# Optimization experiments

Measured on AMD Instinct MI355X. Metric: run time of the kernel, lower is better.

The kernel has to match this reference:

```python
import jax, jax.numpy as jnp
import numpy as np

D_MODEL = 512
NHEAD = 8
HEAD_DIM = D_MODEL // NHEAD
A, B = 1024, 16


def setup_inputs() -> dict:
    key = jax.random.key(0)
    ks = jax.random.split(key, 6)
    s = 1.0 / np.sqrt(D_MODEL)
    return {
        "src": jax.random.normal(ks[0], (A, B, D_MODEL), jnp.float32),
        "asset_relation_bias": jax.random.normal(ks[1], (A, A), jnp.float32) * 0.1,
        "Wq": jax.random.normal(ks[2], (D_MODEL, D_MODEL), jnp.float32) * s,
        "bq": jnp.zeros((D_MODEL,), jnp.float32),
        "Wk": jax.random.normal(ks[3], (D_MODEL, D_MODEL), jnp.float32) * s,
        "bk": jnp.zeros((D_MODEL,), jnp.float32),
        "Wv": jax.random.normal(ks[4], (D_MODEL, D_MODEL), jnp.float32) * s,
        "bv": jnp.zeros((D_MODEL,), jnp.float32),
        "Wo": jax.random.normal(ks[5], (D_MODEL, D_MODEL), jnp.float32) * s,
        "bo": jnp.zeros((D_MODEL,), jnp.float32),
    }


def reference(src, asset_relation_bias, Wq, bq, Wk, bk, Wv, bv, Wo, bo):
    # src: [A, B, H]; attention is over the asset dim A.
    scale = HEAD_DIM ** -0.5

    def proj_heads(x, W, b):
        y = x @ W.T + b                      # [A, B, H]  (torch Linear: x @ W.T + b)
        y = y.reshape(A, B, NHEAD, HEAD_DIM)
        return jnp.transpose(y, (1, 2, 0, 3))  # [B, nh, A, hd]

    q = proj_heads(src, Wq, bq)
    k = proj_heads(src, Wk, bk)
    v = proj_heads(src, Wv, bv)

    logits = jnp.einsum("bnad,bnkd->bnak", q, k) * scale  # [B, nh, A, A]
    logits = logits + asset_relation_bias[None, None]     # additive relation bias
    attn = jax.nn.softmax(logits, axis=-1)                # dropout = identity (eval)
    out = jnp.einsum("bnak,bnkd->bnad", attn, v)          # [B, nh, A, hd]
    out = jnp.transpose(out, (2, 0, 1, 3)).reshape(A, B, D_MODEL)
    out = out @ Wo.T + bo
    return out
```

## Files before the change

kernel.cpp:

```cpp
#include <hip/hip_runtime.h>
#include <hip/hip_bf16.h>

#define A_DIM 1024
#define B_DIM 16
#define DM    512
#define NH    8
#define HD    64

#define LDT 72

typedef short s16x8 __attribute__((ext_vector_type(8)));
typedef float f32x4 __attribute__((ext_vector_type(4)));

static __device__ __forceinline__ unsigned short f2b(float f) {
    __hip_bfloat16 h = __float2bfloat16(f);
    unsigned short u;
    __builtin_memcpy(&u, &h, 2);
    return u;
}
static __device__ __forceinline__ uint2 cvt4(float4 v) {
    __hip_bfloat162 lo = __float22bfloat162_rn(make_float2(v.x, v.y));
    __hip_bfloat162 hi = __float22bfloat162_rn(make_float2(v.z, v.w));
    unsigned int ulo, uhi;
    __builtin_memcpy(&ulo, &lo, 4);
    __builtin_memcpy(&uhi, &hi, 4);
    return make_uint2(ulo, uhi);
}

__global__ __launch_bounds__(256) void qkv_gemm(
    const float* __restrict__ src,
    const float* __restrict__ Wq, const float* __restrict__ bq,
    const float* __restrict__ Wk, const float* __restrict__ bk,
    const float* __restrict__ Wv, const float* __restrict__ bv,
    short* __restrict__ Qb, short* __restrict__ Kb, short* __restrict__ Vb)
{
    __shared__ short As[128 * LDT];
    __shared__ short Bs[128 * LDT];

    const int tid  = threadIdx.x;
    const int wave = tid >> 6, lane = tid & 63;
    const int quad = lane >> 4, l16 = lane & 15;
    const int waveM = (wave >> 1) * 64, waveN = (wave & 1) * 64;
    const int mbase = blockIdx.y * 128;
    const int nbase = blockIdx.x * 128;
    const int mat   = nbase >> 9;
    const float* W    = (mat == 0) ? Wq : (mat == 1) ? Wk : Wv;
    const float* bvec = (mat == 0) ? bq : (mat == 1) ? bk : bv;
    short* dst        = (mat == 0) ? Qb : (mat == 1) ? Kb : Vb;
    const float oscale = (mat == 0) ? 0.125f : 1.0f;
    const int wrow0 = nbase & 511;

    f32x4 acc[4][4];
    #pragma unroll
    for (int i = 0; i < 4; i++)
        #pragma unroll
        for (int j = 0; j < 4; j++)
            acc[i][j] = (f32x4){0.f, 0.f, 0.f, 0.f};

    for (int kb = 0; kb < 8; ++kb) {
        __syncthreads();
        #pragma unroll
        for (int p = 0; p < 8; p++) {
            int chunk = tid + p * 256;
            int row = chunk >> 4, c = chunk & 15;
            float4 a4 = *(const float4*)&src[(mbase + row) * 512 + kb * 64 + c * 4];
            *(uint2*)&As[row * LDT + c * 4] = cvt4(a4);
            float4 w4 = *(const float4*)&W[(wrow0 + row) * 512 + kb * 64 + c * 4];
            *(uint2*)&Bs[row * LDT + c * 4] = cvt4(w4);
        }
        __syncthreads();
        #pragma unroll
        for (int k0i = 0; k0i < 2; k0i++) {
            s16x8 af[4], bf[4];
            #pragma unroll
            for (int mi = 0; mi < 4; mi++)
                af[mi] = *(const s16x8*)&As[(waveM + mi * 16 + l16) * LDT + (k0i * 4 + quad) * 8];
            #pragma unroll
            for (int ni = 0; ni < 4; ni++)
                bf[ni] = *(const s16x8*)&Bs[(waveN + ni * 16 + l16) * LDT + (k0i * 4 + quad) * 8];
            #pragma unroll
            for (int mi = 0; mi < 4; mi++)
                #pragma unroll
                for (int ni = 0; ni < 4; ni++)
                    acc[mi][ni] = __builtin_amdgcn_mfma_f32_16x16x32_bf16(
                        af[mi], bf[ni], acc[mi][ni], 0, 0, 0);
        }
    }

    #pragma unroll
    for (int mi = 0; mi < 4; mi++) {
        #pragma unroll
        for (int ni = 0; ni < 4; ni++) {
            #pragma unroll
            for (int r = 0; r < 4; r++) {
                int t = mbase + waveM + mi * 16 + quad * 4 + r;
                int o = wrow0 + waveN + ni * 16 + l16;
                float v = (acc[mi][ni][r] + bvec[o]) * oscale;
                int a = t >> 4, bb = t & 15, n = o >> 6, d = o & 63;
                dst[((bb * NH + n) * A_DIM + a) * HD + d] = (short)f2b(v);
            }
        }
    }
}

__global__ __launch_bounds__(256) void attn_kernel(
    const short* __restrict__ Qb, const short* __restrict__ Kb,
    const short* __restrict__ Vb, const float* __restrict__ bias,
    short* __restrict__ AO)
{
    __shared__ short Ks[64 * LDT];
    __shared__ short Vt[64 * LDT];
    __shared__ short Ps[4][16 * LDT];

    const int tid  = threadIdx.x;
    const int wave = tid >> 6, lane = tid & 63;
    const int quad = lane >> 4, l16 = lane & 15;
    const int bn = blockIdx.y;
    const int qrow0 = blockIdx.x * 64 + wave * 16;

    const short* Qg = Qb + bn * (A_DIM * HD);
    const short* Kg = Kb + bn * (A_DIM * HD);
    const short* Vg = Vb + bn * (A_DIM * HD);

    s16x8 qf[2];
    #pragma unroll
    for (int k0i = 0; k0i < 2; k0i++)
        qf[k0i] = *(const s16x8*)&Qg[(qrow0 + l16) * HD + k0i * 32 + quad * 8];

    float lsum[4];
    f32x4 of[4];
    #pragma unroll
    for (int r = 0; r < 4; r++) lsum[r] = 0.f;
    #pragma unroll
    for (int db = 0; db < 4; db++) of[db] = (f32x4){0.f, 0.f, 0.f, 0.f};

    for (int kb = 0; kb < 16; ++kb) {
        __syncthreads();
        #pragma unroll
        for (int p = 0; p < 2; p++) {
            int chunk = tid + p * 256;
            int row = chunk >> 3, c = chunk & 7;
            *(s16x8*)&Ks[row * LDT + c * 8] =
                *(const s16x8*)&Kg[(kb * 64 + row) * HD + c * 8];
            s16x8 vv = *(const s16x8*)&Vg[(kb * 64 + row) * HD + c * 8];
            #pragma unroll
            for (int j = 0; j < 8; j++) {
                int d = c * 8 + j;
                Vt[d * LDT + (((row >> 3) ^ c) << 3) + (row & 7)] = vv[j];
            }
        }
        __syncthreads();

        float sv[4][4];
        #pragma unroll
        for (int cb = 0; cb < 4; cb++) {
            f32x4 s = (f32x4){0.f, 0.f, 0.f, 0.f};
            #pragma unroll
            for (int k0i = 0; k0i < 2; k0i++) {
                s16x8 kf = *(const s16x8*)&Ks[(cb * 16 + l16) * LDT + (k0i * 4 + quad) * 8];
                s = __builtin_amdgcn_mfma_f32_16x16x32_bf16(qf[k0i], kf, s, 0, 0, 0);
            }
            #pragma unroll
            for (int r = 0; r < 4; r++) {
                int arow = qrow0 + quad * 4 + r;
                int kcol = kb * 64 + cb * 16 + l16;
                sv[cb][r] = s[r] + bias[arow * A_DIM + kcol];
            }
        }

        #pragma unroll
        for (int r = 0; r < 4; r++) {
            int prow = quad * 4 + r;
            #pragma unroll
            for (int cb = 0; cb < 4; cb++) {
                float pv = __expf(sv[cb][r]);
                lsum[r] += pv;
                Ps[wave][prow * LDT + cb * 16 + l16] = (short)f2b(pv);
            }
        }

        #pragma unroll
        for (int k0i = 0; k0i < 2; k0i++) {
            s16x8 pf = *(const s16x8*)&Ps[wave][l16 * LDT + (k0i * 4 + quad) * 8];
            #pragma unroll
            for (int db = 0; db < 4; db++) {
                int rr = db * 16 + l16;
                s16x8 vf = *(const s16x8*)&Vt[rr * LDT +
                            (((k0i * 4 + quad) ^ (rr >> 3)) << 3)];
                of[db] = __builtin_amdgcn_mfma_f32_16x16x32_bf16(pf, vf, of[db], 0, 0, 0);
            }
        }
    }

    #pragma unroll
    for (int r = 0; r < 4; r++) {
        float ps = lsum[r];
        ps += __shfl_xor(ps, 1);
        ps += __shfl_xor(ps, 2);
        ps += __shfl_xor(ps, 4);
        ps += __shfl_xor(ps, 8);
        lsum[r] = 1.0f / ps;
    }

    const int b = bn >> 3, n = bn & 7;
    #pragma unroll
    for (int db = 0; db < 4; db++) {
        #pragma unroll
        for (int r = 0; r < 4; r++) {
            int a = qrow0 + quad * 4 + r;
            int d = db * 16 + l16;
            float v = of[db][r] * lsum[r];
            AO[(a * B_DIM + b) * DM + n * HD + d] = (short)f2b(v);
        }
    }
}

__global__ __launch_bounds__(256) void out_gemm(
    const short* __restrict__ Xin,
    const float* __restrict__ Wo, const float* __restrict__ bo,
    float* __restrict__ out)
{
    __shared__ short As[128 * LDT];
    __shared__ short Bs[128 * LDT];

    const int tid  = threadIdx.x;
    const int wave = tid >> 6, lane = tid & 63;
    const int quad = lane >> 4, l16 = lane & 15;
    const int waveM = (wave >> 1) * 64, waveN = (wave & 1) * 64;
    const int mbase = blockIdx.y * 128;
    const int nbase = blockIdx.x * 128;

    f32x4 acc[4][4];
    #pragma unroll
    for (int i = 0; i < 4; i++)
        #pragma unroll
        for (int j = 0; j < 4; j++)
            acc[i][j] = (f32x4){0.f, 0.f, 0.f, 0.f};

    for (int kb = 0; kb < 8; ++kb) {
        __syncthreads();
        #pragma unroll
        for (int p = 0; p < 4; p++) {
            int chunk = tid + p * 256;
            int row = chunk >> 3, c = chunk & 7;
            *(s16x8*)&As[row * LDT + c * 8] =
                *(const s16x8*)&Xin[(mbase + row) * 512 + kb * 64 + c * 8];
        }
        #pragma unroll
        for (int p = 0; p < 8; p++) {
            int chunk = tid + p * 256;
            int row = chunk >> 4, c = chunk & 15;
            float4 w4 = *(const float4*)&Wo[(nbase + row) * 512 + kb * 64 + c * 4];
            *(uint2*)&Bs[row * LDT + c * 4] = cvt4(w4);
        }
        __syncthreads();
        #pragma unroll
        for (int k0i = 0; k0i < 2; k0i++) {
            s16x8 af[4], bf[4];
            #pragma unroll
            for (int mi = 0; mi < 4; mi++)
                af[mi] = *(const s16x8*)&As[(waveM + mi * 16 + l16) * LDT + (k0i * 4 + quad) * 8];
            #pragma unroll
            for (int ni = 0; ni < 4; ni++)
                bf[ni] = *(const s16x8*)&Bs[(waveN + ni * 16 + l16) * LDT + (k0i * 4 + quad) * 8];
            #pragma unroll
            for (int mi = 0; mi < 4; mi++)
                #pragma unroll
                for (int ni = 0; ni < 4; ni++)
                    acc[mi][ni] = __builtin_amdgcn_mfma_f32_16x16x32_bf16(
                        af[mi], bf[ni], acc[mi][ni], 0, 0, 0);
        }
    }

    #pragma unroll
    for (int mi = 0; mi < 4; mi++) {
        #pragma unroll
        for (int ni = 0; ni < 4; ni++) {
            #pragma unroll
            for (int r = 0; r < 4; r++) {
                int t = mbase + waveM + mi * 16 + quad * 4 + r;
                int o = nbase + waveN + ni * 16 + l16;
                out[t * 512 + o] = acc[mi][ni][r] + bo[o];
            }
        }
    }
}

extern "C" void kernel_launch(void* const* d_in, const int* in_sizes, int n_in,
                              void* d_out, int out_size, void* d_ws, size_t ws_size,
                              hipStream_t stream) {
    const float* src  = (const float*)d_in[0];
    const float* bias = (const float*)d_in[1];
    const float* Wq   = (const float*)d_in[2];
    const float* bq   = (const float*)d_in[3];
    const float* Wk   = (const float*)d_in[4];
    const float* bk   = (const float*)d_in[5];
    const float* Wv   = (const float*)d_in[6];
    const float* bv   = (const float*)d_in[7];
    const float* Wo   = (const float*)d_in[8];
    const float* bo   = (const float*)d_in[9];

    short* ws = (short*)d_ws;
    short* Qb = ws;
    short* Kb = ws + (size_t)(1 << 23);
    short* Vb = ws + (size_t)(2 << 23);

    const bool big_ws = ws_size >= (size_t)(64u << 20);
    short* AO = big_ws ? (ws + (size_t)3 * (1 << 23))
                       : (short*)d_out;

    qkv_gemm<<<dim3(12, 128), 256, 0, stream>>>(src, Wq, bq, Wk, bk, Wv, bv, Qb, Kb, Vb);
    attn_kernel<<<dim3(16, 128), 256, 0, stream>>>(Qb, Kb, Vb, bias, AO);

    if (big_ws) {
        out_gemm<<<dim3(4, 128), 256, 0, stream>>>(AO, Wo, bo, (float*)d_out);
    } else {
        float* Cs = (float*)d_ws;
        out_gemm<<<dim3(4, 128), 256, 0, stream>>>(AO, Wo, bo, Cs);
        (void)hipMemcpyAsync(d_out, Cs, (size_t)out_size * sizeof(float),
                             hipMemcpyDeviceToDevice, stream);
    }
}
```

Baseline: 251.7 us.

## Use transposing LDS reads for P and V, prefetch next K/V tile into registers

The attention kernel no longer transposes V with scalar element-wise LDS stores. V is stored in a subtiled layout and read with ds_read_b64_tr_b16 transposing loads, and P is written packed as 4-wide bf16 stores and read back the same way. The next K/V tile is also prefetched into registers during compute, so global latency overlaps the current tile. This cuts LDS store count and bank conflicts and hides global loads, at the cost of inline asm, explicit waitcnt and sched barriers that limit compiler scheduling, plus extra registers.

```diff
diff --git a/kernel.cpp b/kernel.cpp
--- a/kernel.cpp
+++ b/kernel.cpp
@@ -10,6 +10,7 @@
 #define LDT 72
 
 typedef short s16x8 __attribute__((ext_vector_type(8)));
+typedef short s16x4 __attribute__((ext_vector_type(4)));
 typedef float f32x4 __attribute__((ext_vector_type(4)));
 
 static __device__ __forceinline__ unsigned short f2b(float f) {
@@ -108,9 +109,9 @@
     const short* __restrict__ Vb, const float* __restrict__ bias,
     short* __restrict__ AO)
 {
-    __shared__ short Ks[64 * LDT];
-    __shared__ short Vt[64 * LDT];
-    __shared__ short Ps[4][16 * LDT];
+    __shared__ __align__(16) short Ks[64 * LDT];
+    __shared__ __align__(16) short Vsub[64 * 64];
+    __shared__ __align__(16) short Pts[4][64 * 16];
 
     const int tid  = threadIdx.x;
     const int wave = tid >> 6, lane = tid & 63;
@@ -127,6 +128,14 @@
     for (int k0i = 0; k0i < 2; k0i++)
         qf[k0i] = *(const s16x8*)&Qg[(qrow0 + l16) * HD + k0i * 32 + quad * 8];
 
+    const int srow = tid >> 3, sc = tid & 7;
+    const short* kld = Kg + srow * HD + sc * 8;
+    const short* vld = Vg + srow * HD + sc * 8;
+
+    const unsigned lane_tr = (unsigned)(quad * 256 + l16 * 8);
+    const unsigned pt_addr = (unsigned)(unsigned long long)&Pts[wave][0] + lane_tr;
+    const unsigned vt_addr = (unsigned)(unsigned long long)&Vsub[0]     + lane_tr;
+
     float lsum[4];
     f32x4 of[4];
     #pragma unroll
@@ -134,22 +143,31 @@
     #pragma unroll
     for (int db = 0; db < 4; db++) of[db] = (f32x4){0.f, 0.f, 0.f, 0.f};
 
+    s16x8 kpre[2], vpre[2];
+    #pragma unroll
+    for (int p = 0; p < 2; p++) {
+        kpre[p] = *(const s16x8*)&kld[p * 32 * HD];
+        vpre[p] = *(const s16x8*)&vld[p * 32 * HD];
+    }
+
     for (int kb = 0; kb < 16; ++kb) {
         __syncthreads();
         #pragma unroll
         for (int p = 0; p < 2; p++) {
-            int chunk = tid + p * 256;
-            int row = chunk >> 3, c = chunk & 7;
-            *(s16x8*)&Ks[row * LDT + c * 8] =
-                *(const s16x8*)&Kg[(kb * 64 + row) * HD + c * 8];
-            s16x8 vv = *(const s16x8*)&Vg[(kb * 64 + row) * HD + c * 8];
-            #pragma unroll
-            for (int j = 0; j < 8; j++) {
-                int d = c * 8 + j;
-                Vt[d * LDT + (((row >> 3) ^ c) << 3) + (row & 7)] = vv[j];
-            }
-        }
-        __syncthreads();
+            int row = srow + p * 32;
+            *(s16x8*)&Ks[row * LDT + sc * 8] = kpre[p];
+            *(s16x8*)&Vsub[(((sc >> 1) * 16 + (row >> 2)) * 64)
+                           + (row & 3) * 16 + (sc & 1) * 8] = vpre[p];
+        }
+        __syncthreads();
+
+        if (kb < 15) {
+            #pragma unroll
+            for (int p = 0; p < 2; p++) {
+                kpre[p] = *(const s16x8*)&kld[((kb + 1) * 64 + p * 32) * HD];
+                vpre[p] = *(const s16x8*)&vld[((kb + 1) * 64 + p * 32) * HD];
+            }
+        }
 
         float sv[4][4];
         #pragma unroll
@@ -169,24 +187,44 @@
         }
 
         #pragma unroll
-        for (int r = 0; r < 4; r++) {
-            int prow = quad * 4 + r;
-            #pragma unroll
-            for (int cb = 0; cb < 4; cb++) {
-                float pv = __expf(sv[cb][r]);
-                lsum[r] += pv;
-                Ps[wave][prow * LDT + cb * 16 + l16] = (short)f2b(pv);
-            }
-        }
-
+        for (int cb = 0; cb < 4; cb++) {
+            float p0 = __expf(sv[cb][0]);
+            float p1 = __expf(sv[cb][1]);
+            float p2 = __expf(sv[cb][2]);
+            float p3 = __expf(sv[cb][3]);
+            lsum[0] += p0; lsum[1] += p1; lsum[2] += p2; lsum[3] += p3;
+            *(uint2*)&Pts[wave][(cb * 4 + (l16 >> 2)) * 64
+                                + (l16 & 3) * 16 + quad * 4] =
+                cvt4(make_float4(p0, p1, p2, p3));
+        }
+
+        asm volatile("s_waitcnt lgkmcnt(0)" ::: "memory");
+
+        s16x4 pl[2], ph[2], vl[2][4], vh[2][4];
         #pragma unroll
         for (int k0i = 0; k0i < 2; k0i++) {
-            s16x8 pf = *(const s16x8*)&Ps[wave][l16 * LDT + (k0i * 4 + quad) * 8];
+            asm volatile("ds_read_b64_tr_b16 %0, %2\n\t"
+                         "ds_read_b64_tr_b16 %1, %2 offset:128"
+                         : "=&v"(pl[k0i]), "=&v"(ph[k0i])
+                         : "v"(pt_addr + (unsigned)(k0i * 1024)));
+            #pragma unroll
+            for (int db = 0; db < 4; db++)
+                asm volatile("ds_read_b64_tr_b16 %0, %2\n\t"
+                             "ds_read_b64_tr_b16 %1, %2 offset:128"
+                             : "=&v"(vl[k0i][db]), "=&v"(vh[k0i][db])
+                             : "v"(vt_addr + (unsigned)(db * 2048 + k0i * 1024)));
+        }
+        asm volatile("s_waitcnt lgkmcnt(0)" ::: "memory");
+        __builtin_amdgcn_sched_barrier(0);
+
+        #pragma unroll
+        for (int k0i = 0; k0i < 2; k0i++) {
+            s16x8 pf = __builtin_shufflevector(pl[k0i], ph[k0i],
+                                               0, 1, 2, 3, 4, 5, 6, 7);
             #pragma unroll
             for (int db = 0; db < 4; db++) {
-                int rr = db * 16 + l16;
-                s16x8 vf = *(const s16x8*)&Vt[rr * LDT +
-                            (((k0i * 4 + quad) ^ (rr >> 3)) << 3)];
+                s16x8 vf = __builtin_shufflevector(vl[k0i][db], vh[k0i][db],
+                                                   0, 1, 2, 3, 4, 5, 6, 7);
                 of[db] = __builtin_amdgcn_mfma_f32_16x16x32_bf16(pf, vf, of[db], 0, 0, 0);
             }
         }
```

Result: slower. 303.8 us (+20.7%).

## Pre-convert src and weights to bf16 and use bf16-input projection GEMMs

Applied to the files above, without the earlier changes.

Adds conversion kernels that turn src and all four weight matrices into bf16 buffers in the workspace once per call. New QKV and output GEMM kernels then load bf16 tiles straight into shared memory instead of converting fp32 on the fly. This halves the global traffic for operands that each GEMM block reads repeatedly and drops the conversion work from the GEMM inner loop. The cost is two extra launches, an extra pass over src, and a larger workspace requirement; if the workspace is too small, the old path is used instead.

```diff
diff --git a/kernel.cpp b/kernel.cpp
--- a/kernel.cpp
+++ b/kernel.cpp
@@ -25,6 +25,106 @@
     __builtin_memcpy(&ulo, &lo, 4);
     __builtin_memcpy(&uhi, &hi, 4);
     return make_uint2(ulo, uhi);
+}
+
+__global__ __launch_bounds__(256) void cvt_src(
+    const float* __restrict__ in, short* __restrict__ out)
+{
+    int i = (blockIdx.x * 256 + threadIdx.x) * 8;
+    float4 a = *(const float4*)&in[i];
+    float4 b = *(const float4*)&in[i + 4];
+    *(uint2*)&out[i]     = cvt4(a);
+    *(uint2*)&out[i + 4] = cvt4(b);
+}
+
+__global__ __launch_bounds__(256) void cvt_w(
+    const float* __restrict__ Wq, const float* __restrict__ Wk,
+    const float* __restrict__ Wv, const float* __restrict__ Wo,
+    short* __restrict__ Wall)
+{
+    int i = blockIdx.x * 256 + threadIdx.x;
+    int mat = i >> 15;
+    const float* W = (mat == 0) ? Wq : (mat == 1) ? Wk : (mat == 2) ? Wv : Wo;
+    int j = (i & 32767) * 8;
+    float4 a = *(const float4*)&W[j];
+    float4 b = *(const float4*)&W[j + 4];
+    *(uint2*)&Wall[mat * (DM * DM) + j]     = cvt4(a);
+    *(uint2*)&Wall[mat * (DM * DM) + j + 4] = cvt4(b);
+}
+
+__global__ __launch_bounds__(256) void qkv_gemm_bf(
+    const short* __restrict__ Sb, const short* __restrict__ Wall,
+    const float* __restrict__ bq, const float* __restrict__ bk,
+    const float* __restrict__ bv,
+    short* __restrict__ Qb, short* __restrict__ Kb, short* __restrict__ Vb)
+{
+    __shared__ short As[128 * LDT];
+    __shared__ short Bs[128 * LDT];
+
+    const int tid  = threadIdx.x;
+    const int wave = tid >> 6, lane = tid & 63;
+    const int quad = lane >> 4, l16 = lane & 15;
+    const int waveM = (wave >> 1) * 64, waveN = (wave & 1) * 64;
+    const int mbase = blockIdx.y * 128;
+    const int nbase = blockIdx.x * 128;
+    const int mat   = nbase >> 9;
+    const short* Wm   = Wall + mat * (DM * DM);
+    const float* bvec = (mat == 0) ? bq : (mat == 1) ? bk : bv;
+    short* dst        = (mat == 0) ? Qb : (mat == 1) ? Kb : Vb;
+    const float oscale = (mat == 0) ? 0.125f : 1.0f;
+    const int wrow0 = nbase & 511;
+
+    f32x4 acc[4][4];
+    #pragma unroll
+    for (int i = 0; i < 4; i++)
+        #pragma unroll
+        for (int j = 0; j < 4; j++)
+            acc[i][j] = (f32x4){0.f, 0.f, 0.f, 0.f};
+
+    for (int kb = 0; kb < 8; ++kb) {
+        __syncthreads();
+        #pragma unroll
+        for (int p = 0; p < 4; p++) {
+            int chunk = tid + p * 256;
+            int row = chunk >> 3, c = chunk & 7;
+            *(s16x8*)&As[row * LDT + c * 8] =
+                *(const s16x8*)&Sb[(mbase + row) * 512 + kb * 64 + c * 8];
+            *(s16x8*)&Bs[row * LDT + c * 8] =
+                *(const s16x8*)&Wm[(wrow0 + row) * 512 + kb * 64 + c * 8];
+        }
+        __syncthreads();
+        #pragma unroll
+        for (int k0i = 0; k0i < 2; k0i++) {
+            s16x8 af[4], bf[4];
+            #pragma unroll
+            for (int mi = 0; mi < 4; mi++)
+                af[mi] = *(const s16x8*)&As[(waveM + mi * 16 + l16) * LDT + (k0i * 4 + quad) * 8];
+            #pragma unroll
+            for (int ni = 0; ni < 4; ni++)
+                bf[ni] = *(const s16x8*)&Bs[(waveN + ni * 16 + l16) * LDT + (k0i * 4 + quad) * 8];
+            #pragma unroll
+            for (int mi = 0; mi < 4; mi++)
+                #pragma unroll
+                for (int ni = 0; ni < 4; ni++)
+                    acc[mi][ni] = __builtin_amdgcn_mfma_f32_16x16x32_bf16(
+                        af[mi], bf[ni], acc[mi][ni], 0, 0, 0);
+        }
+    }
+
+    #pragma unroll
+    for (int mi = 0; mi < 4; mi++) {
+        #pragma unroll
+        for (int ni = 0; ni < 4; ni++) {
+            #pragma unroll
+            for (int r = 0; r < 4; r++) {
+                int t = mbase + waveM + mi * 16 + quad * 4 + r;
+                int o = wrow0 + waveN + ni * 16 + l16;
+                float v = (acc[mi][ni][r] + bvec[o]) * oscale;
+                int a = t >> 4, bb = t & 15, n = o >> 6, d = o & 63;
+                dst[((bb * NH + n) * A_DIM + a) * HD + d] = (short)f2b(v);
+            }
+        }
+    }
 }
 
 __global__ __launch_bounds__(256) void qkv_gemm(
@@ -211,6 +311,72 @@
             int d = db * 16 + l16;
             float v = of[db][r] * lsum[r];
             AO[(a * B_DIM + b) * DM + n * HD + d] = (short)f2b(v);
+        }
+    }
+}
+
+__global__ __launch_bounds__(256) void out_gemm_bf(
+    const short* __restrict__ Xin,
+    const short* __restrict__ Wob, const float* __restrict__ bo,
+    float* __restrict__ out)
+{
+    __shared__ short As[128 * LDT];
+    __shared__ short Bs[128 * LDT];
+
+    const int tid  = threadIdx.x;
+    const int wave = tid >> 6, lane = tid & 63;
+    const int quad = lane >> 4, l16 = lane & 15;
+    const int waveM = (wave >> 1) * 64, waveN = (wave & 1) * 64;
+    const int mbase = blockIdx.y * 128;
+    const int nbase = blockIdx.x * 128;
+
+    f32x4 acc[4][4];
+    #pragma unroll
+    for (int i = 0; i < 4; i++)
+        #pragma unroll
+        for (int j = 0; j < 4; j++)
+            acc[i][j] = (f32x4){0.f, 0.f, 0.f, 0.f};
+
+    for (int kb = 0; kb < 8; ++kb) {
+        __syncthreads();
+        #pragma unroll
+        for (int p = 0; p < 4; p++) {
+            int chunk = tid + p * 256;
+            int row = chunk >> 3, c = chunk & 7;
+            *(s16x8*)&As[row * LDT + c * 8] =
+                *(const s16x8*)&Xin[(mbase + row) * 512 + kb * 64 + c * 8];
+            *(s16x8*)&Bs[row * LDT + c * 8] =
+                *(const s16x8*)&Wob[(nbase + row) * 512 + kb * 64 + c * 8];
+        }
+        __syncthreads();
+        #pragma unroll
+        for (int k0i = 0; k0i < 2; k0i++) {
+            s16x8 af[4], bf[4];
+            #pragma unroll
+            for (int mi = 0; mi < 4; mi++)
+                af[mi] = *(const s16x8*)&As[(waveM + mi * 16 + l16) * LDT + (k0i * 4 + quad) * 8];
+            #pragma unroll
+            for (int ni = 0; ni < 4; ni++)
+                bf[ni] = *(const s16x8*)&Bs[(waveN + ni * 16 + l16) * LDT + (k0i * 4 + quad) * 8];
+            #pragma unroll
+            for (int mi = 0; mi < 4; mi++)
+                #pragma unroll
+                for (int ni = 0; ni < 4; ni++)
+                    acc[mi][ni] = __builtin_amdgcn_mfma_f32_16x16x32_bf16(
+                        af[mi], bf[ni], acc[mi][ni], 0, 0, 0);
+        }
+    }
+
+    #pragma unroll
+    for (int mi = 0; mi < 4; mi++) {
+        #pragma unroll
+        for (int ni = 0; ni < 4; ni++) {
+            #pragma unroll
+            for (int r = 0; r < 4; r++) {
+                int t = mbase + waveM + mi * 16 + quad * 4 + r;
+                int o = nbase + waveN + ni * 16 + l16;
+                out[t * 512 + o] = acc[mi][ni][r] + bo[o];
+            }
         }
     }
 }
@@ -305,19 +471,34 @@
     short* Kb = ws + (size_t)(1 << 23);
     short* Vb = ws + (size_t)(2 << 23);
 
+    const bool big2   = ws_size >= (size_t)(66u << 20);
     const bool big_ws = ws_size >= (size_t)(64u << 20);
-    short* AO = big_ws ? (ws + (size_t)3 * (1 << 23))
-                       : (short*)d_out;
-
-    qkv_gemm<<<dim3(12, 128), 256, 0, stream>>>(src, Wq, bq, Wk, bk, Wv, bv, Qb, Kb, Vb);
-    attn_kernel<<<dim3(16, 128), 256, 0, stream>>>(Qb, Kb, Vb, bias, AO);
-
-    if (big_ws) {
-        out_gemm<<<dim3(4, 128), 256, 0, stream>>>(AO, Wo, bo, (float*)d_out);
+
+    if (big2) {
+        short* Sb   = ws + (size_t)3 * (1 << 23);
+        short* Wall = ws + (size_t)4 * (1 << 23);
+        short* AO   = Sb;
+
+        cvt_src<<<dim3(4096), 256, 0, stream>>>(src, Sb);
+        cvt_w<<<dim3(512), 256, 0, stream>>>(Wq, Wk, Wv, Wo, Wall);
+        qkv_gemm_bf<<<dim3(12, 128), 256, 0, stream>>>(Sb, Wall, bq, bk, bv, Qb, Kb, Vb);
+        attn_kernel<<<dim3(16, 128), 256, 0, stream>>>(Qb, Kb, Vb, bias, AO);
+        out_gemm_bf<<<dim3(4, 128), 256, 0, stream>>>(AO, Wall + 3 * (DM * DM), bo,
+                                                      (float*)d_out);
     } else {
-        float* Cs = (float*)d_ws;
-        out_gemm<<<dim3(4, 128), 256, 0, stream>>>(AO, Wo, bo, Cs);
-        (void)hipMemcpyAsync(d_out, Cs, (size_t)out_size * sizeof(float),
-                             hipMemcpyDeviceToDevice, stream);
-    }
-}
+        short* AO = big_ws ? (ws + (size_t)3 * (1 << 23))
+                           : (short*)d_out;
+
+        qkv_gemm<<<dim3(12, 128), 256, 0, stream>>>(src, Wq, bq, Wk, bk, Wv, bv, Qb, Kb, Vb);
+        attn_kernel<<<dim3(16, 128), 256, 0, stream>>>(Qb, Kb, Vb, bias, AO);
+
+        if (big_ws) {
+            out_gemm<<<dim3(4, 128), 256, 0, stream>>>(AO, Wo, bo, (float*)d_out);
+        } else {
+            float* Cs = (float*)d_ws;
+            out_gemm<<<dim3(4, 128), 256, 0, stream>>>(AO, Wo, bo, Cs);
+            (void)hipMemcpyAsync(d_out, Cs, (size_t)out_size * sizeof(float),
+                                 hipMemcpyDeviceToDevice, stream);
+        }
+    }
+}
```

Result: faster. 241.6 us (-4.0%).
